# Kernel tuning notes

Hardware: AMD Instinct MI355X
Metric: run time of the kernel (lower is better)

The kernel has to match this reference:

```python
import jax, jax.numpy as jnp
import numpy as np

N_NODES = 100000
N_EDGES = 1600000
NFEAT, NHID, NCLASS = 256, 128, 64


def gcn_conv(x, edge_index, edge_weight, W):
    # PyG GCNConv (normalize=False, add_self_loops=False, bias=False):
    # h = x @ W.T; out[i] = sum over edges (j->i) of w_e * h[j]
    h = x @ W.T                                   # [N, out]
    src, dst = edge_index[0], edge_index[1]
    msgs = h[src] * edge_weight[:, None]          # [E, out]
    return jax.ops.segment_sum(msgs, dst, num_segments=x.shape[0])


def setup_inputs() -> dict:
    key = jax.random.key(0)
    ks = jax.random.split(key, 7)
    x = jax.random.normal(ks[0], (N_NODES, NFEAT), dtype=jnp.float32)
    edge_index1 = jax.random.randint(ks[1], (2, N_EDGES), 0, N_NODES, dtype=jnp.int64)
    edge_index2 = jax.random.randint(ks[2], (2, N_EDGES), 0, N_NODES, dtype=jnp.int64)
    edge_weight1 = jax.random.uniform(ks[3], (N_EDGES,), dtype=jnp.float32)
    edge_weight2 = jax.random.uniform(ks[4], (N_EDGES,), dtype=jnp.float32)
    W1 = jax.random.normal(ks[5], (NHID, NFEAT), dtype=jnp.float32) * (1.0 / np.sqrt(NFEAT))
    W2 = jax.random.normal(ks[6], (NCLASS, NHID), dtype=jnp.float32) * (1.0 / np.sqrt(NHID))
    return {"x": x, "edge_index1": edge_index1, "edge_index2": edge_index2,
            "edge_weight1": edge_weight1, "edge_weight2": edge_weight2,
            "W1": W1, "W2": W2}


def reference(x, edge_index1, edge_index2, edge_weight1, edge_weight2, W1, W2):
    h = jax.nn.relu(gcn_conv(x, edge_index1, edge_weight1, W1))
    out = gcn_conv(h, edge_index2, edge_weight2, W2)
    return out
```

## Files before the change

kernel.cpp:

```cpp
#include <hip/hip_runtime.h>

typedef __attribute__((ext_vector_type(8))) short short8;
typedef __attribute__((ext_vector_type(4))) float floatx4;

#define BKT_SHIFT 7
#define BKT_MASK 127
#define CAP 2560

__device__ __forceinline__ ushort f2bf(float f) {
    uint u = __builtin_bit_cast(uint, f);
    uint r = (u + 0x7FFFu + ((u >> 16) & 1u)) >> 16;
    return (ushort)r;
}
__device__ __forceinline__ float bflo(uint h) {
    return __builtin_bit_cast(float, h << 16);
}
__device__ __forceinline__ float bfhi(uint h) {
    return __builtin_bit_cast(float, h & 0xffff0000u);
}

__global__ __launch_bounds__(256) void prep(const uint* __restrict__ ei,
                                            int* __restrict__ flag,
                                            const float* __restrict__ W1,
                                            const float* __restrict__ W2,
                                            ushort* __restrict__ w1b,
                                            ushort* __restrict__ w2b,
                                            int* __restrict__ cntz,
                                            int n1, int n2) {
    if (blockIdx.x == 0 && threadIdx.x < 64) {
        uint v = ei[2 * threadIdx.x + 1];
        unsigned long long b = __ballot(v != 0u);
        if (threadIdx.x == 0) *flag = (b == 0ull) ? 1 : 0;
    }
    int i = blockIdx.x * 256 + threadIdx.x;
    if (i < 2048) cntz[i] = 0;
    if (i < n1) w1b[i] = f2bf(W1[i]);
    else if (i < n1 + n2) w2b[i - n1] = f2bf(W2[i - n1]);
}


__device__ __forceinline__ void dev_cvt(const float* __restrict__ X,
                                        ushort* __restrict__ XB, long n, int bid) {
    long i = ((long)bid * 256 + threadIdx.x) * 8;
    if (i < n) {
        floatx4 a = *(const floatx4*)(X + i);
        floatx4 b = *(const floatx4*)(X + i + 4);
        short8 o;
        #pragma unroll
        for (int j = 0; j < 4; j++) {
            o[j]     = (short)f2bf(a[j]);
            o[4 + j] = (short)f2bf(b[j]);
        }
        *(short8*)(XB + i) = o;
    }
}

__device__ __forceinline__ void dev_bin(int* sm, const void* __restrict__ eidx,
                                        const float* __restrict__ ew,
                                        int* __restrict__ cntg, int2* __restrict__ binA,
                                        int E, int nbk, int nblk, int bid,
                                        const int* __restrict__ flag) {
    int* lc = sm;
    int* lb = sm + 1024;
    int* lo = sm + 2048;
    for (int t = threadIdx.x; t < 1024; t += 256) { lc[t] = 0; lo[t] = 0; }
    __syncthreads();
    int S = (E + nblk - 1) / nblk;
    int s = bid * S, e = min(E, s + S);
    bool f = *flag;
    for (int i = s + threadIdx.x; i < e; i += 256) {
        int dst = f ? (int)((const long long*)eidx)[i + E] : ((const int*)eidx)[i + E];
        atomicAdd(&lc[dst >> BKT_SHIFT], 1);
    }
    __syncthreads();
    for (int t = threadIdx.x; t < nbk; t += 256)
        lb[t] = lc[t] ? atomicAdd(&cntg[t], lc[t]) : 0;
    __syncthreads();
    for (int i = s + threadIdx.x; i < e; i += 256) {
        int src, dst;
        if (f) { const long long* p = (const long long*)eidx; src = (int)p[i]; dst = (int)p[i + E]; }
        else   { const int* p = (const int*)eidx;             src = p[i];      dst = p[i + E]; }
        int bk = dst >> BKT_SHIFT;
        int pos = lb[bk] + atomicAdd(&lo[bk], 1);
        if (pos < CAP)
            binA[(long)bk * CAP + pos] = make_int2(src | ((dst & BKT_MASK) << 24),
                                                   __builtin_bit_cast(int, ew[i]));
    }
}

__device__ __forceinline__ void dev_sort(char* smem, const int2* __restrict__ binA,
                                         const int* __restrict__ cntg,
                                         int2* __restrict__ pairs,
                                         int2* __restrict__ rr, int N, int b) {
    int* hcnt = (int*)smem;
    int* hcur = hcnt + 128;
    int2* ps  = (int2*)(smem + 1024);
    int t = threadIdx.x;
    const long base = (long)b * CAP;
    int n = min(cntg[b], CAP);
    if (t < 128) { hcnt[t] = 0; hcur[t] = 0; }
    __syncthreads();
    for (int i = t; i < n; i += 256)
        atomicAdd(&hcnt[(uint)binA[base + i].x >> 24], 1);
    __syncthreads();
    for (int off = 1; off < 128; off <<= 1) {
        int v = (t >= off && t < 128) ? hcnt[t - off] : 0;
        __syncthreads();
        if (t < 128) hcnt[t] += v;
        __syncthreads();
    }
    if (t < 128) {
        int node = (b << BKT_SHIFT) + t;
        int ex = t ? hcnt[t - 1] : 0;
        if (node < N) rr[node] = make_int2((int)base + ex, (int)base + hcnt[t]);
    }
    __syncthreads();
    for (int i = t; i < n; i += 256) {
        int2 p = binA[base + i];
        int dl = (uint)p.x >> 24;
        int pos = (dl ? hcnt[dl - 1] : 0) + atomicAdd(&hcur[dl], 1);
        ps[pos] = make_int2(p.x & 0x00FFFFFF, p.y);
    }
    __syncthreads();
    for (int j = t; j < n; j += 256) pairs[base + j] = ps[j];
}

template<int K, int NOUT, bool XF32>
__device__ __forceinline__ void dev_gemm(char* xs, const void* __restrict__ Xv,
                                         const ushort* __restrict__ W,
                                         ushort* __restrict__ Y, int N, int bid) {
    constexpr int NT = NOUT / 16;
    constexpr int KS = K / 32;
    constexpr int RB = XF32 ? K * 4 : K * 2;
    const int tid  = threadIdx.x;
    const int lane = tid & 63;
    const int wv   = tid >> 6;
    const int t    = lane & 15;
    const int q    = lane >> 4;
    const int rbase = bid * 64;

    if (XF32) {
        #pragma unroll
        for (int i = 0; i < 16; i++) {
            int rl = wv * 16 + i;
            int grow = rbase + rl;
            if (grow < N) {
                const char* src = (const char*)Xv + (long)grow * RB
                                + ((lane * 16) ^ ((rl & 7) << 5));
                __builtin_amdgcn_global_load_lds(
                    (const __attribute__((address_space(1))) void*)src,
                    (__attribute__((address_space(3))) void*)&xs[rl * RB], 16, 0, 0);
            }
        }
    } else {
        constexpr int LPR = RB / 16;
        constexpr int RPI = 64 / LPR;
        constexpr int NI = 16 / RPI;
        #pragma unroll
        for (int i = 0; i < NI; i++) {
            int rl0 = wv * 16 + i * RPI;
            int grow0 = rbase + rl0;
            if (grow0 < N) {
                int rl = rl0 + lane / LPR;
                const char* src = (const char*)Xv + (long)grow0 * RB + (lane / LPR) * RB
                                + (((lane % LPR) * 16) ^ ((rl & 7) << 5));
                __builtin_amdgcn_global_load_lds(
                    (const __attribute__((address_space(1))) void*)src,
                    (__attribute__((address_space(3))) void*)&xs[rl0 * RB], 16, 0, 0);
            }
        }
    }
    __syncthreads();

    floatx4 acc[NT];
    #pragma unroll
    for (int b = 0; b < NT; b++)
        #pragma unroll
        for (int i = 0; i < 4; i++) acc[b][i] = 0.f;

    const int lrow = wv * 16 + t;
    const char* xrow = &xs[lrow * RB];
    const uint swz = (uint)((t & 7) << 5);

    for (int ks = 0; ks < KS; ks++) {
        short8 af;
        if (XF32) {
            uint off = ((uint)(ks * 128 + q * 32)) ^ swz;
            floatx4 lo = *(const floatx4*)(xrow + off);
            floatx4 hi = *(const floatx4*)(xrow + off + 16);
            #pragma unroll
            for (int j = 0; j < 4; j++) {
                af[j]     = (short)f2bf(lo[j]);
                af[4 + j] = (short)f2bf(hi[j]);
            }
        } else {
            af = *(const short8*)(xrow + (((uint)(ks * 64 + q * 16)) ^ swz));
        }
        #pragma unroll
        for (int nt = 0; nt < NT; nt++) {
            short8 bf = *(const short8*)(W + (long)(nt * 16 + t) * K + ks * 32 + q * 8);
            acc[nt] = __builtin_amdgcn_mfma_f32_16x16x32_bf16(af, bf, acc[nt], 0, 0, 0);
        }
    }

    const int obase = rbase + wv * 16;
    #pragma unroll
    for (int j = 0; j < 4; j++) {
        int orow = obase + q * 4 + j;
        if (orow < N) {
            #pragma unroll
            for (int nt = 0; nt < NT; nt++)
                Y[(long)orow * NOUT + nt * 16 + t] = f2bf(acc[nt][j]);
        }
    }
}

template<int F, bool RELU, bool BF16OUT>
__device__ __forceinline__ void dev_gather(const ushort* __restrict__ H,
                                           const int2* __restrict__ pairs,
                                           const int2* __restrict__ rr,
                                           void* __restrict__ out, int N, int bid) {
    constexpr int L   = F / 2;
    constexpr int LPE = F / 4;
    constexpr int G   = 64 / LPE;
    constexpr int U   = 4;
    int wave = (bid * 256 + (int)threadIdx.x) >> 6;
    int lane = threadIdx.x & 63;
    int node = wave;
    if (node >= N) return;
    const int g  = lane / LPE;
    const int cL = lane % LPE;
    int2 se = rr[node];
    int s = se.x, e = se.y;

    float a0 = 0.f, a1 = 0.f, a2 = 0.f, a3 = 0.f;
    float b0 = 0.f, b1 = 0.f, b2 = 0.f, b3 = 0.f;
    float c0 = 0.f, c1 = 0.f, c2 = 0.f, c3 = 0.f;
    float d0 = 0.f, d1 = 0.f, d2 = 0.f, d3 = 0.f;

    int cnt = e - s;
    int full = cnt / (G * U);
    for (int k = 0; k < full; k++) {
        int idx = s + k * U * G + g;
        int2 p0 = pairs[idx];
        int2 p1 = pairs[idx + G];
        int2 p2 = pairs[idx + 2 * G];
        int2 p3 = pairs[idx + 3 * G];
        uint2 h0 = *(const uint2*)(H + (long)p0.x * F + 4 * cL);
        uint2 h1 = *(const uint2*)(H + (long)p1.x * F + 4 * cL);
        uint2 h2 = *(const uint2*)(H + (long)p2.x * F + 4 * cL);
        uint2 h3 = *(const uint2*)(H + (long)p3.x * F + 4 * cL);
        float w0 = __builtin_bit_cast(float, p0.y), w1 = __builtin_bit_cast(float, p1.y);
        float w2 = __builtin_bit_cast(float, p2.y), w3 = __builtin_bit_cast(float, p3.y);
        a0 += w0 * bflo(h0.x);  a1 += w0 * bfhi(h0.x);
        a2 += w0 * bflo(h0.y);  a3 += w0 * bfhi(h0.y);
        b0 += w1 * bflo(h1.x);  b1 += w1 * bfhi(h1.x);
        b2 += w1 * bflo(h1.y);  b3 += w1 * bfhi(h1.y);
        c0 += w2 * bflo(h2.x);  c1 += w2 * bfhi(h2.x);
        c2 += w2 * bflo(h2.y);  c3 += w2 * bfhi(h2.y);
        d0 += w3 * bflo(h3.x);  d1 += w3 * bfhi(h3.x);
        d2 += w3 * bflo(h3.y);  d3 += w3 * bfhi(h3.y);
    }
    for (int idx = s + full * U * G + g; idx < e; idx += G) {
        int2 p = pairs[idx];
        uint2 h = *(const uint2*)(H + (long)p.x * F + 4 * cL);
        float w = __builtin_bit_cast(float, p.y);
        a0 += w * bflo(h.x);  a1 += w * bfhi(h.x);
        a2 += w * bflo(h.y);  a3 += w * bfhi(h.y);
    }
    float r0 = (a0 + b0) + (c0 + d0);
    float r1 = (a1 + b1) + (c1 + d1);
    float r2 = (a2 + b2) + (c2 + d2);
    float r3 = (a3 + b3) + (c3 + d3);
    #pragma unroll
    for (int m = LPE; m < 64; m <<= 1) {
        r0 += __shfl_xor(r0, m);
        r1 += __shfl_xor(r1, m);
        r2 += __shfl_xor(r2, m);
        r3 += __shfl_xor(r3, m);
    }
    if (g == 0) {
        if (BF16OUT) {
            if (RELU) {
                r0 = fmaxf(r0, 0.f); r1 = fmaxf(r1, 0.f);
                r2 = fmaxf(r2, 0.f); r3 = fmaxf(r3, 0.f);
            }
            uint2 pk;
            pk.x = (uint)f2bf(r0) | ((uint)f2bf(r1) << 16);
            pk.y = (uint)f2bf(r2) | ((uint)f2bf(r3) << 16);
            *(uint2*)((uint*)out + (long)node * L + 2 * cL) = pk;
        } else {
            float4 r; r.x = r0; r.y = r1; r.z = r2; r.w = r3;
            *(float4*)((float*)out + (long)node * F + 4 * cL) = r;
        }
    }
}


__global__ __launch_bounds__(256) void fuse_cvt_bin(const float* __restrict__ X,
                                                    ushort* __restrict__ XB, long n,
                                                    const void* __restrict__ eidx,
                                                    const float* __restrict__ ew,
                                                    int* __restrict__ cntg,
                                                    int2* __restrict__ binA, int E, int nbk,
                                                    const int* __restrict__ flag) {
    __shared__ __align__(16) int sm[3072];
    if (blockIdx.x < 256) dev_bin(sm, eidx, ew, cntg, binA, E, nbk, 256, blockIdx.x, flag);
    else dev_cvt(X, XB, n, blockIdx.x - 256);
}

__global__ __launch_bounds__(256) void bin_only(const void* __restrict__ eidx,
                                                const float* __restrict__ ew,
                                                int* __restrict__ cntg,
                                                int2* __restrict__ binA, int E, int nbk,
                                                const int* __restrict__ flag) {
    __shared__ __align__(16) int sm[3072];
    dev_bin(sm, eidx, ew, cntg, binA, E, nbk, (int)gridDim.x, blockIdx.x, flag);
}

template<int K, int NOUT, bool XF32>
__global__ __launch_bounds__(256) void fuse_gemm_sort(const void* __restrict__ Xv,
                                                      const ushort* __restrict__ W,
                                                      ushort* __restrict__ Y, int N, int gb,
                                                      const int2* __restrict__ binA,
                                                      const int* __restrict__ cntg,
                                                      int2* __restrict__ pairs,
                                                      int2* __restrict__ rr) {
    constexpr int RB = XF32 ? K * 4 : K * 2;
    constexpr int GS = 64 * RB;
    constexpr int SS = 1024 + CAP * 8;
    constexpr int SM = GS > SS ? GS : SS;
    __shared__ __align__(16) char smem[SM];
    if ((int)blockIdx.x < gb) dev_gemm<K, NOUT, XF32>(smem, Xv, W, Y, N, blockIdx.x);
    else dev_sort(smem, binA, cntg, pairs, rr, N, blockIdx.x - gb);
}

template<int F, bool RELU, bool BF16OUT>
__global__ __launch_bounds__(256) void fuse_gather_bin(const ushort* __restrict__ H,
                                                       const int2* __restrict__ pairs,
                                                       const int2* __restrict__ rr,
                                                       void* __restrict__ out, int N,
                                                       const void* __restrict__ eidx,
                                                       const float* __restrict__ ew,
                                                       int* __restrict__ cntg,
                                                       int2* __restrict__ binA, int E, int nbk,
                                                       const int* __restrict__ flag, int binblk) {
    __shared__ __align__(16) int sm[3072];
    if ((int)blockIdx.x < binblk)
        dev_bin(sm, eidx, ew, cntg, binA, E, nbk, binblk, blockIdx.x, flag);
    else
        dev_gather<F, RELU, BF16OUT>(H, pairs, rr, out, N, blockIdx.x - binblk);
}

extern "C" void kernel_launch(void* const* d_in, const int* in_sizes, int n_in,
                              void* d_out, int out_size, void* d_ws, size_t ws_size,
                              hipStream_t stream) {
    const float* x   = (const float*)d_in[0];
    const void*  ei1 = d_in[1];
    const void*  ei2 = d_in[2];
    const float* ew1 = (const float*)d_in[3];
    const float* ew2 = (const float*)d_in[4];
    const float* W1  = (const float*)d_in[5];
    const float* W2  = (const float*)d_in[6];

    const int N = in_sizes[0] / 256;
    const int E = in_sizes[3];
    const int NBK = (N + BKT_MASK) >> BKT_SHIFT;

    const size_t SZ_F   = (size_t)N * 128 * 2;
    const size_t SZ_XB  = (size_t)N * 256 * 2;
    const size_t SZ_BIN = (size_t)NBK * CAP * 8;
    const size_t SZ_TAIL = (size_t)N * 8 + 2 * 4096 + 128 * 256 * 2 + 64 * 128 * 2 + 256;
    const bool bfp = ws_size >= SZ_F + SZ_XB + 2 * SZ_BIN + SZ_TAIL;

    char* ws = (char*)d_ws;
    size_t off = 0;
    ushort* XW = (ushort*)(ws + off); off += SZ_F;
    ushort* XB = nullptr;
    ushort* hbuf;
    if (bfp) { XB = (ushort*)(ws + off); hbuf = XB; off += SZ_XB; }
    else     { hbuf = (ushort*)(ws + off); off += SZ_F; }
    int2* binA  = (int2*)(ws + off); off += SZ_BIN;
    int2* pairs = (int2*)(ws + off); off += SZ_BIN;
    int2* rr    = (int2*)(ws + off); off += (size_t)N * 8;
    int*  cnt1  = (int*) (ws + off); off += 4096;
    int*  cnt2  = (int*) (ws + off); off += 4096;
    ushort* w1b = (ushort*)(ws + off); off += 128 * 256 * 2;
    ushort* w2b = (ushort*)(ws + off); off += 64 * 128 * 2;
    int*  flag  = (int*) (ws + off);
    ushort* H2  = XW;

    const int gb = (N + 63) / 64;
    const int gab = (N + 3) / 4;

    prep<<<160, 256, 0, stream>>>((const uint*)ei1, flag, W1, W2, w1b, w2b,
                                  cnt1, 128 * 256, 64 * 128);

    if (bfp) {
        long n = (long)N * 256;
        int cvb = (int)((n / 8 + 255) / 256);
        fuse_cvt_bin<<<256 + cvb, 256, 0, stream>>>(x, XB, n, ei1, ew1, cnt1,
                                                    binA, E, NBK, flag);
        fuse_gemm_sort<256, 128, false><<<gb + NBK, 256, 0, stream>>>(
            XB, w1b, XW, N, gb, binA, cnt1, pairs, rr);
    } else {
        bin_only<<<256, 256, 0, stream>>>(ei1, ew1, cnt1, binA, E, NBK, flag);
        fuse_gemm_sort<256, 128, true><<<gb + NBK, 256, 0, stream>>>(
            x, w1b, XW, N, gb, binA, cnt1, pairs, rr);
    }

    fuse_gather_bin<128, true, true><<<256 + gab, 256, 0, stream>>>(
        XW, pairs, rr, hbuf, N, ei2, ew2, cnt2, binA, E, NBK, flag, 256);

    fuse_gemm_sort<128, 64, false><<<gb + NBK, 256, 0, stream>>>(
        hbuf, w2b, H2, N, gb, binA, cnt2, pairs, rr);

    fuse_gather_bin<64, false, false><<<gab, 256, 0, stream>>>(
        H2, pairs, rr, d_out, N, ei2, ew2, cnt2, binA, E, NBK, flag, 0);
}
```

Baseline: 472.0 us.

## Bin layer-2 edges alongside layer-1 binning into a separate buffer

Layer-2 edge binning moves into the first binning kernel and writes to its own bin buffer when the workspace is large enough. The first gather kernel then no longer carries the extra binning blocks. The aim is to overlap both binning passes with the input conversion and shorten the critical path of the layer-1 gather. In exchange it uses an extra bin buffer of workspace and puts more load on the first kernel.

```diff
diff --git a/kernel.cpp b/kernel.cpp
--- a/kernel.cpp
+++ b/kernel.cpp
@@ -297,25 +297,42 @@
 }
 
 
-__global__ __launch_bounds__(256) void fuse_cvt_bin(const float* __restrict__ X,
-                                                    ushort* __restrict__ XB, long n,
-                                                    const void* __restrict__ eidx,
-                                                    const float* __restrict__ ew,
-                                                    int* __restrict__ cntg,
-                                                    int2* __restrict__ binA, int E, int nbk,
-                                                    const int* __restrict__ flag) {
+__global__ __launch_bounds__(256) void fuse_cvt_bin2(const float* __restrict__ X,
+                                                     ushort* __restrict__ XB, long n,
+                                                     const void* __restrict__ e1,
+                                                     const float* __restrict__ wg1,
+                                                     int* __restrict__ cnt1,
+                                                     int2* __restrict__ binA1,
+                                                     const void* __restrict__ e2,
+                                                     const float* __restrict__ wg2,
+                                                     int* __restrict__ cnt2,
+                                                     int2* __restrict__ binA2,
+                                                     int E, int nbk,
+                                                     const int* __restrict__ flag,
+                                                     int bin2blk) {
     __shared__ __align__(16) int sm[3072];
-    if (blockIdx.x < 256) dev_bin(sm, eidx, ew, cntg, binA, E, nbk, 256, blockIdx.x, flag);
-    else dev_cvt(X, XB, n, blockIdx.x - 256);
-}
-
-__global__ __launch_bounds__(256) void bin_only(const void* __restrict__ eidx,
-                                                const float* __restrict__ ew,
-                                                int* __restrict__ cntg,
-                                                int2* __restrict__ binA, int E, int nbk,
-                                                const int* __restrict__ flag) {
+    int bid = blockIdx.x;
+    if (bid < 256) dev_bin(sm, e1, wg1, cnt1, binA1, E, nbk, 256, bid, flag);
+    else if (bid < 256 + bin2blk)
+        dev_bin(sm, e2, wg2, cnt2, binA2, E, nbk, bin2blk, bid - 256, flag);
+    else dev_cvt(X, XB, n, bid - 256 - bin2blk);
+}
+
+__global__ __launch_bounds__(256) void bins_only(const void* __restrict__ e1,
+                                                 const float* __restrict__ wg1,
+                                                 int* __restrict__ cnt1,
+                                                 int2* __restrict__ binA1,
+                                                 const void* __restrict__ e2,
+                                                 const float* __restrict__ wg2,
+                                                 int* __restrict__ cnt2,
+                                                 int2* __restrict__ binA2,
+                                                 int E, int nbk,
+                                                 const int* __restrict__ flag,
+                                                 int bin2blk) {
     __shared__ __align__(16) int sm[3072];
-    dev_bin(sm, eidx, ew, cntg, binA, E, nbk, (int)gridDim.x, blockIdx.x, flag);
+    int bid = blockIdx.x;
+    if (bid < 256) dev_bin(sm, e1, wg1, cnt1, binA1, E, nbk, 256, bid, flag);
+    else dev_bin(sm, e2, wg2, cnt2, binA2, E, nbk, bin2blk, bid - 256, flag);
 }
 
 template<int K, int NOUT, bool XF32>
@@ -371,7 +388,10 @@
     const size_t SZ_XB  = (size_t)N * 256 * 2;
     const size_t SZ_BIN = (size_t)NBK * CAP * 8;
     const size_t SZ_TAIL = (size_t)N * 8 + 2 * 4096 + 128 * 256 * 2 + 64 * 128 * 2 + 256;
-    const bool bfp = ws_size >= SZ_F + SZ_XB + 2 * SZ_BIN + SZ_TAIL;
+
+    const bool bfp  = ws_size >= SZ_F + SZ_XB + 2 * SZ_BIN + SZ_TAIL;
+    const size_t base_need = (bfp ? SZ_F + SZ_XB : 2 * SZ_F) + 2 * SZ_BIN + SZ_TAIL;
+    const bool sep2 = ws_size >= base_need + SZ_BIN;
 
     char* ws = (char*)d_ws;
     size_t off = 0;
@@ -382,6 +402,8 @@
     else     { hbuf = (ushort*)(ws + off); off += SZ_F; }
     int2* binA  = (int2*)(ws + off); off += SZ_BIN;
     int2* pairs = (int2*)(ws + off); off += SZ_BIN;
+    int2* binA2 = binA;
+    if (sep2) { binA2 = (int2*)(ws + off); off += SZ_BIN; }
     int2* rr    = (int2*)(ws + off); off += (size_t)N * 8;
     int*  cnt1  = (int*) (ws + off); off += 4096;
     int*  cnt2  = (int*) (ws + off); off += 4096;
@@ -392,6 +414,7 @@
 
     const int gb = (N + 63) / 64;
     const int gab = (N + 3) / 4;
+    const int b2 = sep2 ? 256 : 0;
 
     prep<<<160, 256, 0, stream>>>((const uint*)ei1, flag, W1, W2, w1b, w2b,
                                   cnt1, 128 * 256, 64 * 128);
@@ -399,22 +422,24 @@
     if (bfp) {
         long n = (long)N * 256;
         int cvb = (int)((n / 8 + 255) / 256);
-        fuse_cvt_bin<<<256 + cvb, 256, 0, stream>>>(x, XB, n, ei1, ew1, cnt1,
-                                                    binA, E, NBK, flag);
+        fuse_cvt_bin2<<<256 + b2 + cvb, 256, 0, stream>>>(
+            x, XB, n, ei1, ew1, cnt1, binA, ei2, ew2, cnt2, binA2, E, NBK, flag, b2);
         fuse_gemm_sort<256, 128, false><<<gb + NBK, 256, 0, stream>>>(
             XB, w1b, XW, N, gb, binA, cnt1, pairs, rr);
     } else {
-        bin_only<<<256, 256, 0, stream>>>(ei1, ew1, cnt1, binA, E, NBK, flag);
+        bins_only<<<256 + b2, 256, 0, stream>>>(
+            ei1, ew1, cnt1, binA, ei2, ew2, cnt2, binA2, E, NBK, flag, b2);
         fuse_gemm_sort<256, 128, true><<<gb + NBK, 256, 0, stream>>>(
             x, w1b, XW, N, gb, binA, cnt1, pairs, rr);
     }
 
-    fuse_gather_bin<128, true, true><<<256 + gab, 256, 0, stream>>>(
-        XW, pairs, rr, hbuf, N, ei2, ew2, cnt2, binA, E, NBK, flag, 256);
+    const int d4bin = sep2 ? 0 : 256;
+    fuse_gather_bin<128, true, true><<<d4bin + gab, 256, 0, stream>>>(
+        XW, pairs, rr, hbuf, N, ei2, ew2, cnt2, binA2, E, NBK, flag, d4bin);
 
     fuse_gemm_sort<128, 64, false><<<gb + NBK, 256, 0, stream>>>(
-        hbuf, w2b, H2, N, gb, binA, cnt2, pairs, rr);
+        hbuf, w2b, H2, N, gb, binA2, cnt2, pairs, rr);
 
     fuse_gather_bin<64, false, false><<<gab, 256, 0, stream>>>(
-        H2, pairs, rr, d_out, N, ei2, ew2, cnt2, binA, E, NBK, flag, 0);
-}
+        H2, pairs, rr, d_out, N, ei2, ew2, cnt2, binA2, E, NBK, flag, 0);
+}
```

After: 457.2 us. -3.1%, faster.
